# Optimization experiments

Hardware: AMD Instinct MI355X
Metric: run time of the kernel (lower is better)

## Reference

```python
import jax, jax.numpy as jnp
import numpy as np

N_NODES = 50000
N_EDGES = 600000
IN_DIM = 128
HID_DIM = 128
OUT_DIM = 128
N_GRAPHS = 64


def _glorot(key, shape):
    lim = np.sqrt(6.0 / (shape[0] + shape[1]))
    return jax.random.uniform(key, shape, jnp.float32, -lim, lim)


def setup_inputs() -> dict:
    key = jax.random.key(0)
    ks = jax.random.split(key, 8)
    h = jax.random.normal(ks[0], (N_NODES, IN_DIM), jnp.float32)
    src = jax.random.randint(ks[1], (N_EDGES,), 0, N_NODES, jnp.int64)
    dst = jax.random.randint(ks[2], (N_EDGES,), 0, N_NODES, jnp.int64)
    graph_ids = jnp.sort(jax.random.randint(ks[3], (N_NODES,), 0, N_GRAPHS, jnp.int64))
    W1 = _glorot(ks[4], (IN_DIM, HID_DIM)); b1 = jnp.zeros((HID_DIM,), jnp.float32)
    W2 = _glorot(ks[5], (HID_DIM, HID_DIM)); b2 = jnp.zeros((HID_DIM,), jnp.float32)
    W3 = _glorot(ks[6], (HID_DIM, OUT_DIM)); b3 = jnp.zeros((OUT_DIM,), jnp.float32)
    return {"h": h, "src": src, "dst": dst, "graph_ids": graph_ids,
            "W1": W1, "b1": b1, "W2": W2, "b2": b2, "W3": W3, "b3": b3,
            "n_graphs": N_GRAPHS}


def _graph_conv(h, src, dst, norm_src, norm_dst, W, b):
    # DGL GraphConv, norm='both': D_dst^{-1/2} A^T D_src^{-1/2} h W + b
    m = h * norm_src[:, None]                                   # [N, d]
    agg = jax.ops.segment_sum(m[src], dst, num_segments=h.shape[0])  # [N, d]
    return (agg * norm_dst[:, None]) @ W + b


def reference(h, src, dst, graph_ids, W1, b1, W2, b2, W3, b3, n_graphs):
    n = h.shape[0]
    ones = jnp.ones((src.shape[0],), h.dtype)
    out_deg = jnp.clip(jax.ops.segment_sum(ones, src, num_segments=n), 1.0)
    in_deg = jnp.clip(jax.ops.segment_sum(ones, dst, num_segments=n), 1.0)
    norm_src = out_deg ** -0.5
    norm_dst = in_deg ** -0.5

    x = jax.nn.relu(_graph_conv(h, src, dst, norm_src, norm_dst, W1, b1))
    x = jax.nn.relu(_graph_conv(x, src, dst, norm_src, norm_dst, W2, b2))
    x = jax.nn.relu(_graph_conv(x, src, dst, norm_src, norm_dst, W3, b3))

    # dgl.mean_nodes: per-graph mean over nodes
    gsum = jax.ops.segment_sum(x, graph_ids, num_segments=n_graphs)          # [G, d]
    gcnt = jax.ops.segment_sum(jnp.ones((n,), x.dtype), graph_ids, num_segments=n_graphs)
    return gsum / jnp.clip(gcnt, 1.0)[:, None]
```

## Files before the change

kernel.cpp:

```cpp
#include <hip/hip_runtime.h>
#include <hip/hip_fp16.h>


#define DIM 128
#define GRAPHS 64

typedef _Float16 half8 __attribute__((ext_vector_type(8)));
typedef _Float16 half4 __attribute__((ext_vector_type(4)));
typedef float floatx4 __attribute__((ext_vector_type(4)));

#define HIST_R 4
#define HIST_S 64
#define NPR 12500
#define LDSW (NPR / 2)

__global__ __launch_bounds__(256) void k_hist(const int* __restrict__ src,
                                              const int* __restrict__ dst,
                                              unsigned* __restrict__ partial, int E) {
    __shared__ unsigned hist[LDSW];
    int b = blockIdx.x;
    int a = b / (HIST_R * HIST_S);
    int r = (b / HIST_S) % HIST_R;
    int s = b % HIST_S;
    const int* arr = a ? dst : src;
    for (int i = threadIdx.x; i < LDSW; i += 256) hist[i] = 0;
    __syncthreads();
    int chunk = (E + HIST_S - 1) / HIST_S;
    int e0 = s * chunk;
    int e1 = min(e0 + chunk, E);
    unsigned base = (unsigned)(r * NPR);
    for (int i = e0 + threadIdx.x; i < e1; i += 256) {
        unsigned n = (unsigned)arr[i] - base;
        if (n < NPR) atomicAdd(&hist[n >> 1], 1u << ((n & 1) * 16));
    }
    __syncthreads();
    unsigned* outp = partial + ((size_t)(a * HIST_R + r) * HIST_S + s) * LDSW;
    for (int i = threadIdx.x; i < LDSW; i += 256) outp[i] = hist[i];
}

__global__ __launch_bounds__(256) void k_hist_merge(const unsigned* __restrict__ partial,
                                                    float* __restrict__ ns,
                                                    float* __restrict__ nd,
                                                    int* __restrict__ inc,
                                                    int* __restrict__ bsum, int N) {
    __shared__ int sred[256];
    int nb = (N + 255) / 256;
    int isDst = (blockIdx.x < nb) ? 1 : 0;
    int cb = isDst ? blockIdx.x : blockIdx.x - nb;
    int n = cb * 256 + threadIdx.x;
    int deg = 0;
    if (n < N) {
        int a = isDst ? 1 : 0;
        int r = n / NPR;
        int w = (n % NPR) >> 1;
        int field = (n & 1) * 16;
        const unsigned* p = partial + ((size_t)(a * HIST_R + r) * HIST_S) * LDSW + w;
        unsigned sum = 0;
#pragma unroll
        for (int s = 0; s < HIST_S; ++s) sum += p[(size_t)s * LDSW];
        deg = (int)((sum >> field) & 0xFFFFu);
        float nrm = rsqrtf(fmaxf((float)deg, 1.0f));
        if (isDst) { nd[n] = nrm; inc[n] = deg; }
        else       { ns[n] = nrm; }
    }
    if (isDst) {
        sred[threadIdx.x] = deg;
        __syncthreads();
        for (int off = 128; off > 0; off >>= 1) {
            if (threadIdx.x < off) sred[threadIdx.x] += sred[threadIdx.x + off];
            __syncthreads();
        }
        if (threadIdx.x == 0) bsum[cb] = sred[0];
    }
}

__global__ __launch_bounds__(256) void k_scan_write(const int* __restrict__ inc,
                                                    const int* __restrict__ bsum,
                                                    const unsigned* __restrict__ partial,
                                                    int* __restrict__ row_ptr,
                                                    int* __restrict__ cur,
                                                    float* __restrict__ gsum, int N) {
    __shared__ int sb[256];
    __shared__ int s[256];
    __shared__ int exs[256];
    int nb = (N + 255) / 256;
    int t = threadIdx.x;

    int bv = (t < nb) ? bsum[t] : 0;
    sb[t] = bv;
    __syncthreads();
    for (int off = 1; off < 256; off <<= 1) {
        int u = (t >= off) ? sb[t - off] : 0;
        __syncthreads();
        sb[t] += u;
        __syncthreads();
    }
    int excl = sb[t] - bv;
    __syncthreads();
    sb[t] = excl;
    __syncthreads();
    int blockBase = sb[blockIdx.x];

    int B = blockIdx.x * 256;
    int i = B + t;
    int v = (i < N) ? inc[i] : 0;
    s[t] = v;
    __syncthreads();
    for (int off = 1; off < 256; off <<= 1) {
        int u = (t >= off) ? s[t - off] : 0;
        __syncthreads();
        s[t] += u;
        __syncthreads();
    }
    int ex = blockBase + s[t] - v;
    exs[t] = ex;
    if (i < N) row_ptr[i] = ex;
    if (i == N - 1) row_ptr[N] = ex + v;
    if (blockIdx.x == 0) {
        for (int j = t; j < GRAPHS * DIM; j += 256) gsum[j] = 0.0f;
    }
    __syncthreads();

    if (t < 128) {
        int n0 = B + 2 * t;
        if (n0 < N) {
            int r = n0 / NPR;
            int w = (n0 % NPR) >> 1;
            const unsigned* p = partial + ((size_t)(HIST_R + r) * HIST_S) * LDSW + w;
            int run0 = exs[2 * t];
            int run1 = exs[2 * t + 1];
            int* c = cur + (size_t)r * HIST_S * NPR + 2 * w;
#pragma unroll
            for (int sl = 0; sl < HIST_S; ++sl) {
                c[(size_t)sl * NPR + 0] = run0;
                c[(size_t)sl * NPR + 1] = run1;
                unsigned hv = p[(size_t)sl * LDSW];
                run0 += (int)(hv & 0xFFFFu);
                run1 += (int)(hv >> 16);
            }
        }
    }
}

__global__ __launch_bounds__(256) void k_fill2(const int* __restrict__ src,
                                               const int* __restrict__ dst,
                                               const int* __restrict__ cur,
                                               int* __restrict__ csr, int E) {
    __shared__ int lcur[NPR];
    int r = blockIdx.x / HIST_S;
    int s = blockIdx.x % HIST_S;
    const int* cs = cur + (size_t)(r * HIST_S + s) * NPR;
    for (int i = threadIdx.x; i < NPR; i += 256) lcur[i] = cs[i];
    __syncthreads();
    int chunk = (E + HIST_S - 1) / HIST_S;
    int e0 = s * chunk;
    int e1 = min(e0 + chunk, E);
    unsigned base = (unsigned)(r * NPR);
    for (int i = e0 + threadIdx.x; i < e1; i += 256) {
        unsigned d = (unsigned)dst[i] - base;
        if (d < NPR) {
            int p = atomicAdd(&lcur[d], 1);
            csr[p] = src[i];
        }
    }
}

__global__ void k_prep(const float4* __restrict__ h, const float* __restrict__ ns,
                       uint2* __restrict__ A,
                       const float* __restrict__ W1, const float* __restrict__ W2,
                       const float* __restrict__ W3, _Float16* __restrict__ Wt1,
                       _Float16* __restrict__ Wt2, _Float16* __restrict__ Wt3, int N) {
    int i = blockIdx.x * blockDim.x + threadIdx.x;
    int nf4 = N * 32;
    if (i < nf4) {
        int n = i >> 5;
        float s = ns[n];
        float4 v = h[i];
        __half2 p0 = __floats2half2_rn(v.x * s, v.y * s);
        __half2 p1 = __floats2half2_rn(v.z * s, v.w * s);
        uint2 o;
        o.x = *(unsigned*)&p0;
        o.y = *(unsigned*)&p1;
        A[i] = o;
    } else {
        int j = i - nf4;
        if (j < 3 * 16384) {
            int which = j >> 14;
            int local = j & 16383;
            int k = local >> 7;
            int n = local & 127;
            const float* W = (which == 0) ? W1 : (which == 1) ? W2 : W3;
            _Float16* Wt = (which == 0) ? Wt1 : (which == 1) ? Wt2 : Wt3;
            Wt[(size_t)n * DIM + k] = (_Float16)W[local];
        }
    }
}

__global__ __launch_bounds__(256) void k_agg(const uint4* __restrict__ A,
                                             const int* __restrict__ row_ptr,
                                             const int* __restrict__ csr,
                                             const float* __restrict__ nd,
                                             uint4* __restrict__ Bh, int N) {
    int gtid = blockIdx.x * blockDim.x + threadIdx.x;
    int node = gtid >> 6;
    int lane = threadIdx.x & 63;
    if (node >= N) return;
    int e0 = row_ptr[node];
    int e1 = row_ptr[node + 1];
    int grp = lane >> 4;
    int l16 = lane & 15;
    float acc[8];
#pragma unroll
    for (int k = 0; k < 8; ++k) acc[k] = 0.0f;

    for (int base = e0; base < e1; base += 32) {
        int vl = csr[min(base + (lane & 31), e1 - 1)];
        uint4 u[8];
#pragma unroll
        for (int j = 0; j < 8; ++j) {
            int idx = __shfl(vl, 4 * j + grp);
            u[j] = A[(size_t)idx * 16 + l16];
        }
#pragma unroll
        for (int j = 0; j < 8; ++j) {
            if (base + 4 * j + grp < e1) {
                __half2 h0 = *(__half2*)&u[j].x;
                __half2 h1 = *(__half2*)&u[j].y;
                __half2 h2 = *(__half2*)&u[j].z;
                __half2 h3 = *(__half2*)&u[j].w;
                float2 f0 = __half22float2(h0);
                float2 f1 = __half22float2(h1);
                float2 f2 = __half22float2(h2);
                float2 f3 = __half22float2(h3);
                acc[0] += f0.x; acc[1] += f0.y;
                acc[2] += f1.x; acc[3] += f1.y;
                acc[4] += f2.x; acc[5] += f2.y;
                acc[6] += f3.x; acc[7] += f3.y;
            }
        }
    }

#pragma unroll
    for (int k = 0; k < 8; ++k) {
        float v = acc[k];
        v += __shfl_xor(v, 16);
        v += __shfl_xor(v, 32);
        acc[k] = v;
    }

    if (grp == 0) {
        float s = nd[node];
        __half2 p0 = __floats2half2_rn(acc[0] * s, acc[1] * s);
        __half2 p1 = __floats2half2_rn(acc[2] * s, acc[3] * s);
        __half2 p2 = __floats2half2_rn(acc[4] * s, acc[5] * s);
        __half2 p3 = __floats2half2_rn(acc[6] * s, acc[7] * s);
        uint4 o;
        o.x = *(unsigned*)&p0;
        o.y = *(unsigned*)&p1;
        o.z = *(unsigned*)&p2;
        o.w = *(unsigned*)&p3;
        Bh[(size_t)node * 16 + l16] = o;
    }
}

template <bool SCALE_NS>
__global__ __launch_bounds__(256) void k_gemm_t(
    const _Float16* __restrict__ Bin, const _Float16* __restrict__ Wt,
    const float* __restrict__ bias, const float* __restrict__ ns,
    _Float16* __restrict__ Xout, int N) {
    int tid = threadIdx.x;
    int wave = tid >> 6;
    int lane = tid & 63;
    int quad = lane >> 4;
    int l16 = lane & 15;
    int node = blockIdx.x * 64 + wave * 16 + l16;

    half8 b[4];
#pragma unroll
    for (int q = 0; q < 4; ++q) {
        if (node < N) {
            b[q] = *(const half8*)&Bin[(size_t)node * DIM + q * 32 + quad * 8];
        } else {
            b[q] = half8{0, 0, 0, 0, 0, 0, 0, 0};
        }
    }

    floatx4 acc[8];
#pragma unroll
    for (int c = 0; c < 8; ++c) acc[c] = floatx4{0.f, 0.f, 0.f, 0.f};

#pragma unroll
    for (int c = 0; c < 8; ++c) {
#pragma unroll
        for (int q = 0; q < 4; ++q) {
            half8 a = *(const half8*)&Wt[(size_t)(c * 16 + l16) * DIM + q * 32 + quad * 8];
            acc[c] = __builtin_amdgcn_mfma_f32_16x16x32_f16(a, b[q], acc[c], 0, 0, 0);
        }
    }

    if (node < N) {
        float s = SCALE_NS ? ns[node] : 1.0f;
#pragma unroll
        for (int c = 0; c < 8; ++c) {
            float4 b4 = *(const float4*)&bias[c * 16 + quad * 4];
            half4 o;
            o[0] = (_Float16)(fmaxf(acc[c][0] + b4.x, 0.0f) * s);
            o[1] = (_Float16)(fmaxf(acc[c][1] + b4.y, 0.0f) * s);
            o[2] = (_Float16)(fmaxf(acc[c][2] + b4.z, 0.0f) * s);
            o[3] = (_Float16)(fmaxf(acc[c][3] + b4.w, 0.0f) * s);
            *(half4*)&Xout[(size_t)node * DIM + c * 16 + quad * 4] = o;
        }
    }
}

#define PBINS 8
__global__ __launch_bounds__(256) void k_gemm_pool(
    const _Float16* __restrict__ Bin, const _Float16* __restrict__ Wt,
    const float* __restrict__ bias, const int* __restrict__ gid,
    float* __restrict__ gsum, int N) {
    __shared__ float lsum[PBINS * DIM];
    int tid = threadIdx.x;
    for (int i = tid; i < PBINS * DIM; i += 256) lsum[i] = 0.0f;
    int wave = tid >> 6;
    int lane = tid & 63;
    int quad = lane >> 4;
    int l16 = lane & 15;
    int r0 = blockIdx.x * 64;
    int node = r0 + wave * 16 + l16;
    int nodec = min(node, N - 1);

    half8 b[4];
#pragma unroll
    for (int q = 0; q < 4; ++q) {
        if (node < N) {
            b[q] = *(const half8*)&Bin[(size_t)node * DIM + q * 32 + quad * 8];
        } else {
            b[q] = half8{0, 0, 0, 0, 0, 0, 0, 0};
        }
    }

    floatx4 acc[8];
#pragma unroll
    for (int c = 0; c < 8; ++c) acc[c] = floatx4{0.f, 0.f, 0.f, 0.f};
    __syncthreads();

#pragma unroll
    for (int c = 0; c < 8; ++c) {
#pragma unroll
        for (int q = 0; q < 4; ++q) {
            half8 a = *(const half8*)&Wt[(size_t)(c * 16 + l16) * DIM + q * 32 + quad * 8];
            acc[c] = __builtin_amdgcn_mfma_f32_16x16x32_f16(a, b[q], acc[c], 0, 0, 0);
        }
    }

    int g = gid[nodec];
    int g0b = gid[r0];
    int gEb = gid[min(r0 + 63, N - 1)];
    bool ldsPath = (gEb - g0b) < PBINS;
    int gF = __shfl(g, 0);
    int gL = __shfl(g, 15);
    bool uni = (gF == gL);
    float valid = (node < N) ? 1.0f : 0.0f;

#pragma unroll
    for (int c = 0; c < 8; ++c) {
        float4 b4 = *(const float4*)&bias[c * 16 + quad * 4];
        float bv[4] = {b4.x, b4.y, b4.z, b4.w};
#pragma unroll
        for (int r = 0; r < 4; ++r) {
            float v = fmaxf(acc[c][r] + bv[r], 0.0f) * valid;
            int f = c * 16 + quad * 4 + r;
            if (ldsPath) {
                if (uni) {
                    v += __shfl_xor(v, 1);
                    v += __shfl_xor(v, 2);
                    v += __shfl_xor(v, 4);
                    v += __shfl_xor(v, 8);
                    if (l16 == 0) atomicAdd(&lsum[(gF - g0b) * DIM + f], v);
                } else {
                    if (node < N) atomicAdd(&lsum[(g - g0b) * DIM + f], v);
                }
            } else {
                if (node < N) atomicAdd(&gsum[(size_t)g * DIM + f], v);
            }
        }
    }
    __syncthreads();
    if (ldsPath) {
        int ng = gEb - g0b + 1;
        for (int i = tid; i < ng * DIM; i += 256) {
            float sv = lsum[i];
            if (sv != 0.0f) atomicAdd(&gsum[(size_t)g0b * DIM + i], sv);
        }
    }
}

__global__ void k_finalize(const float* __restrict__ gsum, const int* __restrict__ gid,
                           float* __restrict__ out, int N, int G) {
    int i = blockIdx.x * blockDim.x + threadIdx.x;
    if (i < G * DIM) {
        int g = i >> 7;
        int lo = 0, hi = N;
        while (lo < hi) { int m = (lo + hi) >> 1; if (gid[m] < g) lo = m + 1; else hi = m; }
        int lo2 = lo, hi2 = N;
        while (lo2 < hi2) { int m = (lo2 + hi2) >> 1; if (gid[m] < g + 1) lo2 = m + 1; else hi2 = m; }
        float c = fmaxf((float)(lo2 - lo), 1.0f);
        out[i] = gsum[i] / c;
    }
}

extern "C" void kernel_launch(void* const* d_in, const int* in_sizes, int n_in,
                              void* d_out, int out_size, void* d_ws, size_t ws_size,
                              hipStream_t stream) {
    const float* h   = (const float*)d_in[0];
    const int*   src = (const int*)d_in[1];
    const int*   dst = (const int*)d_in[2];
    const int*   gid = (const int*)d_in[3];
    const float* W1  = (const float*)d_in[4];
    const float* b1  = (const float*)d_in[5];
    const float* W2  = (const float*)d_in[6];
    const float* b2  = (const float*)d_in[7];
    const float* W3  = (const float*)d_in[8];
    const float* b3  = (const float*)d_in[9];

    const int N = in_sizes[0] / DIM;
    const int E = in_sizes[1];
    const int G = GRAPHS;
    float* out = (float*)d_out;

    char* ws = (char*)d_ws;
    size_t off = 0;
    auto alloc = [&](size_t bytes) -> void* {
        void* p = ws + off;
        off += (bytes + 255) & ~(size_t)255;
        return p;
    };
    const int nb = (N + 255) / 256;
    uint2* Ah0     = (uint2*)alloc((size_t)N * DIM * 2);
    uint2* Ah1     = (uint2*)alloc((size_t)N * DIM * 2);
    uint2* Bh      = (uint2*)alloc((size_t)N * DIM * 2);
    _Float16* X3   = (_Float16*)alloc((size_t)N * DIM * 2);
    _Float16* Wt1  = (_Float16*)alloc((size_t)DIM * DIM * 2);
    _Float16* Wt2  = (_Float16*)alloc((size_t)DIM * DIM * 2);
    _Float16* Wt3  = (_Float16*)alloc((size_t)DIM * DIM * 2);
    float* ns      = (float*)alloc((size_t)N * 4);
    float* nd      = (float*)alloc((size_t)N * 4);
    int*   inc     = (int*)alloc((size_t)N * 4);
    unsigned* partial = (unsigned*)alloc((size_t)2 * HIST_R * HIST_S * LDSW * 4);
    int*   cur     = (int*)alloc((size_t)HIST_R * HIST_S * NPR * 4);
    int*   row_ptr = (int*)alloc((size_t)(N + 1) * 4);
    int*   csr     = (int*)alloc((size_t)E * 4);
    float* gsum    = (float*)alloc((size_t)G * DIM * 4);
    int*   bsum    = (int*)alloc((size_t)nb * 4);
    (void)X3;

    k_hist<<<2 * HIST_R * HIST_S, 256, 0, stream>>>(src, dst, partial, E);
    k_hist_merge<<<2 * nb, 256, 0, stream>>>(partial, ns, nd, inc, bsum, N);
    k_scan_write<<<nb, 256, 0, stream>>>(inc, bsum, partial, row_ptr, cur, gsum, N);
    k_fill2<<<HIST_R * HIST_S, 256, 0, stream>>>(src, dst, cur, csr, E);

    int prepThreads = N * 32 + 3 * 16384;
    k_prep<<<(prepThreads + 255) / 256, 256, 0, stream>>>((const float4*)h, ns, Ah0,
                                                          W1, W2, W3, Wt1, Wt2, Wt3, N);

    int aggBlocks  = (N * 64 + 255) / 256;
    int gemmBlocks = (N + 63) / 64;

    k_agg<<<aggBlocks, 256, 0, stream>>>((const uint4*)Ah0, row_ptr, csr, nd, (uint4*)Bh, N);
    k_gemm_t<true><<<gemmBlocks, 256, 0, stream>>>((const _Float16*)Bh, Wt1, b1, ns, (_Float16*)Ah1, N);
    k_agg<<<aggBlocks, 256, 0, stream>>>((const uint4*)Ah1, row_ptr, csr, nd, (uint4*)Bh, N);
    k_gemm_t<true><<<gemmBlocks, 256, 0, stream>>>((const _Float16*)Bh, Wt2, b2, ns, (_Float16*)Ah0, N);
    k_agg<<<aggBlocks, 256, 0, stream>>>((const uint4*)Ah0, row_ptr, csr, nd, (uint4*)Bh, N);
    k_gemm_pool<<<gemmBlocks, 256, 0, stream>>>((const _Float16*)Bh, Wt3, b3, gid, gsum, N);

    k_finalize<<<(G * DIM + 255) / 256, 256, 0, stream>>>(gsum, gid, out, N, G);
}
```

Baseline: 310.3 us.

## Split node features into 32-wide slices and aggregate each slice separately

Stores node feature matrices as four feature-slice planes of 32 halves per node, and runs the aggregation kernel once per slice. Each slice's gather working set is a quarter of the full matrix, so the random neighbor reads are intended to hit in L2 more often. The GEMM kernels read and write the sliced layout. In exchange, the edge list and row pointers are read four times, and there are four times as many aggregation launches and waves.

```diff
diff --git a/kernel.cpp b/kernel.cpp
--- a/kernel.cpp
+++ b/kernel.cpp
@@ -174,6 +174,7 @@
     int nf4 = N * 32;
     if (i < nf4) {
         int n = i >> 5;
+        int f4 = i & 31;
         float s = ns[n];
         float4 v = h[i];
         __half2 p0 = __floats2half2_rn(v.x * s, v.y * s);
@@ -181,7 +182,9 @@
         uint2 o;
         o.x = *(unsigned*)&p0;
         o.y = *(unsigned*)&p1;
-        A[i] = o;
+        int q = f4 >> 3;
+        int slot = f4 & 7;
+        A[(size_t)q * N * 8 + (size_t)n * 8 + slot] = o;
     } else {
         int j = i - nf4;
         if (j < 3 * 16384) {
@@ -196,70 +199,54 @@
     }
 }
 
-__global__ __launch_bounds__(256) void k_agg(const uint4* __restrict__ A,
+__global__ __launch_bounds__(256) void k_agg(const uint2* __restrict__ Aq,
                                              const int* __restrict__ row_ptr,
                                              const int* __restrict__ csr,
                                              const float* __restrict__ nd,
-                                             uint4* __restrict__ Bh, int N) {
+                                             uint2* __restrict__ Bq, int N) {
     int gtid = blockIdx.x * blockDim.x + threadIdx.x;
     int node = gtid >> 6;
     int lane = threadIdx.x & 63;
     if (node >= N) return;
     int e0 = row_ptr[node];
     int e1 = row_ptr[node + 1];
-    int grp = lane >> 4;
-    int l16 = lane & 15;
-    float acc[8];
-#pragma unroll
-    for (int k = 0; k < 8; ++k) acc[k] = 0.0f;
+    int grp = lane >> 3;
+    int l8 = lane & 7;
+    float a0 = 0.f, a1 = 0.f, a2 = 0.f, a3 = 0.f;
 
     for (int base = e0; base < e1; base += 32) {
         int vl = csr[min(base + (lane & 31), e1 - 1)];
-        uint4 u[8];
-#pragma unroll
-        for (int j = 0; j < 8; ++j) {
-            int idx = __shfl(vl, 4 * j + grp);
-            u[j] = A[(size_t)idx * 16 + l16];
-        }
-#pragma unroll
-        for (int j = 0; j < 8; ++j) {
-            if (base + 4 * j + grp < e1) {
+        uint2 u[4];
+#pragma unroll
+        for (int j = 0; j < 4; ++j) {
+            int idx = __shfl(vl, 8 * j + grp);
+            u[j] = Aq[(size_t)idx * 8 + l8];
+        }
+#pragma unroll
+        for (int j = 0; j < 4; ++j) {
+            if (base + 8 * j + grp < e1) {
                 __half2 h0 = *(__half2*)&u[j].x;
                 __half2 h1 = *(__half2*)&u[j].y;
-                __half2 h2 = *(__half2*)&u[j].z;
-                __half2 h3 = *(__half2*)&u[j].w;
                 float2 f0 = __half22float2(h0);
                 float2 f1 = __half22float2(h1);
-                float2 f2 = __half22float2(h2);
-                float2 f3 = __half22float2(h3);
-                acc[0] += f0.x; acc[1] += f0.y;
-                acc[2] += f1.x; acc[3] += f1.y;
-                acc[4] += f2.x; acc[5] += f2.y;
-                acc[6] += f3.x; acc[7] += f3.y;
+                a0 += f0.x; a1 += f0.y; a2 += f1.x; a3 += f1.y;
             }
         }
     }
 
-#pragma unroll
-    for (int k = 0; k < 8; ++k) {
-        float v = acc[k];
-        v += __shfl_xor(v, 16);
-        v += __shfl_xor(v, 32);
-        acc[k] = v;
-    }
+    a0 += __shfl_xor(a0, 8);  a0 += __shfl_xor(a0, 16); a0 += __shfl_xor(a0, 32);
+    a1 += __shfl_xor(a1, 8);  a1 += __shfl_xor(a1, 16); a1 += __shfl_xor(a1, 32);
+    a2 += __shfl_xor(a2, 8);  a2 += __shfl_xor(a2, 16); a2 += __shfl_xor(a2, 32);
+    a3 += __shfl_xor(a3, 8);  a3 += __shfl_xor(a3, 16); a3 += __shfl_xor(a3, 32);
 
     if (grp == 0) {
         float s = nd[node];
-        __half2 p0 = __floats2half2_rn(acc[0] * s, acc[1] * s);
-        __half2 p1 = __floats2half2_rn(acc[2] * s, acc[3] * s);
-        __half2 p2 = __floats2half2_rn(acc[4] * s, acc[5] * s);
-        __half2 p3 = __floats2half2_rn(acc[6] * s, acc[7] * s);
-        uint4 o;
+        __half2 p0 = __floats2half2_rn(a0 * s, a1 * s);
+        __half2 p1 = __floats2half2_rn(a2 * s, a3 * s);
+        uint2 o;
         o.x = *(unsigned*)&p0;
         o.y = *(unsigned*)&p1;
-        o.z = *(unsigned*)&p2;
-        o.w = *(unsigned*)&p3;
-        Bh[(size_t)node * 16 + l16] = o;
+        Bq[(size_t)node * 8 + l8] = o;
     }
 }
 
@@ -274,12 +261,13 @@
     int quad = lane >> 4;
     int l16 = lane & 15;
     int node = blockIdx.x * 64 + wave * 16 + l16;
+    size_t QS = (size_t)N * 32;
 
     half8 b[4];
 #pragma unroll
     for (int q = 0; q < 4; ++q) {
         if (node < N) {
-            b[q] = *(const half8*)&Bin[(size_t)node * DIM + q * 32 + quad * 8];
+            b[q] = *(const half8*)&Bin[q * QS + (size_t)node * 32 + quad * 8];
         } else {
             b[q] = half8{0, 0, 0, 0, 0, 0, 0, 0};
         }
@@ -308,7 +296,8 @@
             o[1] = (_Float16)(fmaxf(acc[c][1] + b4.y, 0.0f) * s);
             o[2] = (_Float16)(fmaxf(acc[c][2] + b4.z, 0.0f) * s);
             o[3] = (_Float16)(fmaxf(acc[c][3] + b4.w, 0.0f) * s);
-            *(half4*)&Xout[(size_t)node * DIM + c * 16 + quad * 4] = o;
+            int f0 = c * 16 + quad * 4;
+            *(half4*)&Xout[(f0 >> 5) * QS + (size_t)node * 32 + (f0 & 31)] = o;
         }
     }
 }
@@ -328,12 +317,13 @@
     int r0 = blockIdx.x * 64;
     int node = r0 + wave * 16 + l16;
     int nodec = min(node, N - 1);
+    size_t QS = (size_t)N * 32;
 
     half8 b[4];
 #pragma unroll
     for (int q = 0; q < 4; ++q) {
         if (node < N) {
-            b[q] = *(const half8*)&Bin[(size_t)node * DIM + q * 32 + quad * 8];
+            b[q] = *(const half8*)&Bin[q * QS + (size_t)node * 32 + quad * 8];
         } else {
             b[q] = half8{0, 0, 0, 0, 0, 0, 0, 0};
         }
@@ -439,7 +429,6 @@
     uint2* Ah0     = (uint2*)alloc((size_t)N * DIM * 2);
     uint2* Ah1     = (uint2*)alloc((size_t)N * DIM * 2);
     uint2* Bh      = (uint2*)alloc((size_t)N * DIM * 2);
-    _Float16* X3   = (_Float16*)alloc((size_t)N * DIM * 2);
     _Float16* Wt1  = (_Float16*)alloc((size_t)DIM * DIM * 2);
     _Float16* Wt2  = (_Float16*)alloc((size_t)DIM * DIM * 2);
     _Float16* Wt3  = (_Float16*)alloc((size_t)DIM * DIM * 2);
@@ -452,7 +441,6 @@
     int*   csr     = (int*)alloc((size_t)E * 4);
     float* gsum    = (float*)alloc((size_t)G * DIM * 4);
     int*   bsum    = (int*)alloc((size_t)nb * 4);
-    (void)X3;
 
     k_hist<<<2 * HIST_R * HIST_S, 256, 0, stream>>>(src, dst, partial, E);
     k_hist_merge<<<2 * nb, 256, 0, stream>>>(partial, ns, nd, inc, bsum, N);
@@ -465,12 +453,16 @@
 
     int aggBlocks  = (N * 64 + 255) / 256;
     int gemmBlocks = (N + 63) / 64;
-
-    k_agg<<<aggBlocks, 256, 0, stream>>>((const uint4*)Ah0, row_ptr, csr, nd, (uint4*)Bh, N);
+    size_t QU2 = (size_t)N * 8;
+
+    for (int q = 0; q < 4; ++q)
+        k_agg<<<aggBlocks, 256, 0, stream>>>(Ah0 + q * QU2, row_ptr, csr, nd, Bh + q * QU2, N);
     k_gemm_t<true><<<gemmBlocks, 256, 0, stream>>>((const _Float16*)Bh, Wt1, b1, ns, (_Float16*)Ah1, N);
-    k_agg<<<aggBlocks, 256, 0, stream>>>((const uint4*)Ah1, row_ptr, csr, nd, (uint4*)Bh, N);
+    for (int q = 0; q < 4; ++q)
+        k_agg<<<aggBlocks, 256, 0, stream>>>(Ah1 + q * QU2, row_ptr, csr, nd, Bh + q * QU2, N);
     k_gemm_t<true><<<gemmBlocks, 256, 0, stream>>>((const _Float16*)Bh, Wt2, b2, ns, (_Float16*)Ah0, N);
-    k_agg<<<aggBlocks, 256, 0, stream>>>((const uint4*)Ah0, row_ptr, csr, nd, (uint4*)Bh, N);
+    for (int q = 0; q < 4; ++q)
+        k_agg<<<aggBlocks, 256, 0, stream>>>(Ah0 + q * QU2, row_ptr, csr, nd, Bh + q * QU2, N);
     k_gemm_pool<<<gemmBlocks, 256, 0, stream>>>((const _Float16*)Bh, Wt3, b3, gid, gsum, N);
 
     k_finalize<<<(G * DIM + 255) / 256, 256, 0, stream>>>(gsum, gid, out, N, G);
```

New measurement: 429.8 us. +38.5%, slower.

## Replace LDS-partitioned histogram CSR build with global atomic degree count and fill

Applied to the files above, without the earlier changes.

Swaps the multi-pass, LDS-partitioned degree histogram and per-slice cursor scheme for simple global atomics: one pass counts src and dst degrees, a scan produces row_ptr and a single cursor array, and a fill kernel scatters src indices with global atomicAdd on the cursor. This removes the large partial-histogram and cursor buffers and the 64-way serial cursor writes. In exchange it relies on contended global atomics and makes CSR neighbor order nondeterministic, which may change floating-point summation order and gather locality in the aggregation kernels.

```diff
diff --git a/kernel.cpp b/kernel.cpp
--- a/kernel.cpp
+++ b/kernel.cpp
@@ -9,40 +9,22 @@
 typedef _Float16 half4 __attribute__((ext_vector_type(4)));
 typedef float floatx4 __attribute__((ext_vector_type(4)));
 
-#define HIST_R 4
-#define HIST_S 64
-#define NPR 12500
-#define LDSW (NPR / 2)
-
-__global__ __launch_bounds__(256) void k_hist(const int* __restrict__ src,
-                                              const int* __restrict__ dst,
-                                              unsigned* __restrict__ partial, int E) {
-    __shared__ unsigned hist[LDSW];
-    int b = blockIdx.x;
-    int a = b / (HIST_R * HIST_S);
-    int r = (b / HIST_S) % HIST_R;
-    int s = b % HIST_S;
-    const int* arr = a ? dst : src;
-    for (int i = threadIdx.x; i < LDSW; i += 256) hist[i] = 0;
-    __syncthreads();
-    int chunk = (E + HIST_S - 1) / HIST_S;
-    int e0 = s * chunk;
-    int e1 = min(e0 + chunk, E);
-    unsigned base = (unsigned)(r * NPR);
-    for (int i = e0 + threadIdx.x; i < e1; i += 256) {
-        unsigned n = (unsigned)arr[i] - base;
-        if (n < NPR) atomicAdd(&hist[n >> 1], 1u << ((n & 1) * 16));
-    }
-    __syncthreads();
-    unsigned* outp = partial + ((size_t)(a * HIST_R + r) * HIST_S + s) * LDSW;
-    for (int i = threadIdx.x; i < LDSW; i += 256) outp[i] = hist[i];
-}
-
-__global__ __launch_bounds__(256) void k_hist_merge(const unsigned* __restrict__ partial,
-                                                    float* __restrict__ ns,
-                                                    float* __restrict__ nd,
-                                                    int* __restrict__ inc,
-                                                    int* __restrict__ bsum, int N) {
+__global__ __launch_bounds__(256) void k_deg(const int* __restrict__ src,
+                                             const int* __restrict__ dst,
+                                             int* __restrict__ degs,
+                                             int* __restrict__ degd, int E) {
+    int e = blockIdx.x * 256 + threadIdx.x;
+    if (e < E) {
+        atomicAdd(&degs[src[e]], 1);
+        atomicAdd(&degd[dst[e]], 1);
+    }
+}
+
+__global__ __launch_bounds__(256) void k_bsum(const int* __restrict__ degs,
+                                              const int* __restrict__ degd,
+                                              float* __restrict__ ns,
+                                              float* __restrict__ nd,
+                                              int* __restrict__ bsum, int N) {
     __shared__ int sred[256];
     int nb = (N + 255) / 256;
     int isDst = (blockIdx.x < nb) ? 1 : 0;
@@ -50,18 +32,9 @@
     int n = cb * 256 + threadIdx.x;
     int deg = 0;
     if (n < N) {
-        int a = isDst ? 1 : 0;
-        int r = n / NPR;
-        int w = (n % NPR) >> 1;
-        int field = (n & 1) * 16;
-        const unsigned* p = partial + ((size_t)(a * HIST_R + r) * HIST_S) * LDSW + w;
-        unsigned sum = 0;
-#pragma unroll
-        for (int s = 0; s < HIST_S; ++s) sum += p[(size_t)s * LDSW];
-        deg = (int)((sum >> field) & 0xFFFFu);
+        deg = isDst ? degd[n] : degs[n];
         float nrm = rsqrtf(fmaxf((float)deg, 1.0f));
-        if (isDst) { nd[n] = nrm; inc[n] = deg; }
-        else       { ns[n] = nrm; }
+        if (isDst) nd[n] = nrm; else ns[n] = nrm;
     }
     if (isDst) {
         sred[threadIdx.x] = deg;
@@ -74,15 +47,13 @@
     }
 }
 
-__global__ __launch_bounds__(256) void k_scan_write(const int* __restrict__ inc,
-                                                    const int* __restrict__ bsum,
-                                                    const unsigned* __restrict__ partial,
-                                                    int* __restrict__ row_ptr,
-                                                    int* __restrict__ cur,
-                                                    float* __restrict__ gsum, int N) {
+__global__ __launch_bounds__(256) void k_scan(const int* __restrict__ degd,
+                                              const int* __restrict__ bsum,
+                                              int* __restrict__ row_ptr,
+                                              int* __restrict__ cursor,
+                                              float* __restrict__ gsum, int N) {
     __shared__ int sb[256];
     __shared__ int s[256];
-    __shared__ int exs[256];
     int nb = (N + 255) / 256;
     int t = threadIdx.x;
 
@@ -103,7 +74,7 @@
 
     int B = blockIdx.x * 256;
     int i = B + t;
-    int v = (i < N) ? inc[i] : 0;
+    int v = (i < N) ? degd[i] : 0;
     s[t] = v;
     __syncthreads();
     for (int off = 1; off < 256; off <<= 1) {
@@ -113,55 +84,22 @@
         __syncthreads();
     }
     int ex = blockBase + s[t] - v;
-    exs[t] = ex;
-    if (i < N) row_ptr[i] = ex;
+    if (i < N) { row_ptr[i] = ex; cursor[i] = ex; }
     if (i == N - 1) row_ptr[N] = ex + v;
     if (blockIdx.x == 0) {
         for (int j = t; j < GRAPHS * DIM; j += 256) gsum[j] = 0.0f;
     }
-    __syncthreads();
-
-    if (t < 128) {
-        int n0 = B + 2 * t;
-        if (n0 < N) {
-            int r = n0 / NPR;
-            int w = (n0 % NPR) >> 1;
-            const unsigned* p = partial + ((size_t)(HIST_R + r) * HIST_S) * LDSW + w;
-            int run0 = exs[2 * t];
-            int run1 = exs[2 * t + 1];
-            int* c = cur + (size_t)r * HIST_S * NPR + 2 * w;
-#pragma unroll
-            for (int sl = 0; sl < HIST_S; ++sl) {
-                c[(size_t)sl * NPR + 0] = run0;
-                c[(size_t)sl * NPR + 1] = run1;
-                unsigned hv = p[(size_t)sl * LDSW];
-                run0 += (int)(hv & 0xFFFFu);
-                run1 += (int)(hv >> 16);
-            }
-        }
-    }
-}
-
-__global__ __launch_bounds__(256) void k_fill2(const int* __restrict__ src,
-                                               const int* __restrict__ dst,
-                                               const int* __restrict__ cur,
-                                               int* __restrict__ csr, int E) {
-    __shared__ int lcur[NPR];
-    int r = blockIdx.x / HIST_S;
-    int s = blockIdx.x % HIST_S;
-    const int* cs = cur + (size_t)(r * HIST_S + s) * NPR;
-    for (int i = threadIdx.x; i < NPR; i += 256) lcur[i] = cs[i];
-    __syncthreads();
-    int chunk = (E + HIST_S - 1) / HIST_S;
-    int e0 = s * chunk;
-    int e1 = min(e0 + chunk, E);
-    unsigned base = (unsigned)(r * NPR);
-    for (int i = e0 + threadIdx.x; i < e1; i += 256) {
-        unsigned d = (unsigned)dst[i] - base;
-        if (d < NPR) {
-            int p = atomicAdd(&lcur[d], 1);
-            csr[p] = src[i];
-        }
+}
+
+__global__ __launch_bounds__(256) void k_fill(const int* __restrict__ src,
+                                              const int* __restrict__ dst,
+                                              int* __restrict__ cursor,
+                                              int* __restrict__ csr, int E) {
+    int e = blockIdx.x * 256 + threadIdx.x;
+    if (e < E) {
+        int d = dst[e];
+        int p = atomicAdd(&cursor[d], 1);
+        csr[p] = src[e];
     }
 }
 
@@ -439,25 +377,27 @@
     uint2* Ah0     = (uint2*)alloc((size_t)N * DIM * 2);
     uint2* Ah1     = (uint2*)alloc((size_t)N * DIM * 2);
     uint2* Bh      = (uint2*)alloc((size_t)N * DIM * 2);
-    _Float16* X3   = (_Float16*)alloc((size_t)N * DIM * 2);
     _Float16* Wt1  = (_Float16*)alloc((size_t)DIM * DIM * 2);
     _Float16* Wt2  = (_Float16*)alloc((size_t)DIM * DIM * 2);
     _Float16* Wt3  = (_Float16*)alloc((size_t)DIM * DIM * 2);
     float* ns      = (float*)alloc((size_t)N * 4);
     float* nd      = (float*)alloc((size_t)N * 4);
-    int*   inc     = (int*)alloc((size_t)N * 4);
-    unsigned* partial = (unsigned*)alloc((size_t)2 * HIST_R * HIST_S * LDSW * 4);
-    int*   cur     = (int*)alloc((size_t)HIST_R * HIST_S * NPR * 4);
+    int*   deg2    = (int*)alloc((size_t)2 * N * 4);
     int*   row_ptr = (int*)alloc((size_t)(N + 1) * 4);
+    int*   cursor  = (int*)alloc((size_t)N * 4);
     int*   csr     = (int*)alloc((size_t)E * 4);
     float* gsum    = (float*)alloc((size_t)G * DIM * 4);
     int*   bsum    = (int*)alloc((size_t)nb * 4);
-    (void)X3;
-
-    k_hist<<<2 * HIST_R * HIST_S, 256, 0, stream>>>(src, dst, partial, E);
-    k_hist_merge<<<2 * nb, 256, 0, stream>>>(partial, ns, nd, inc, bsum, N);
-    k_scan_write<<<nb, 256, 0, stream>>>(inc, bsum, partial, row_ptr, cur, gsum, N);
-    k_fill2<<<HIST_R * HIST_S, 256, 0, stream>>>(src, dst, cur, csr, E);
+    int*   degs = deg2;
+    int*   degd = deg2 + N;
+
+    int edgeBlocks = (E + 255) / 256;
+
+    hipMemsetAsync(deg2, 0, (size_t)2 * N * 4, stream);
+    k_deg<<<edgeBlocks, 256, 0, stream>>>(src, dst, degs, degd, E);
+    k_bsum<<<2 * nb, 256, 0, stream>>>(degs, degd, ns, nd, bsum, N);
+    k_scan<<<nb, 256, 0, stream>>>(degd, bsum, row_ptr, cursor, gsum, N);
+    k_fill<<<edgeBlocks, 256, 0, stream>>>(src, dst, cursor, csr, E);
 
     int prepThreads = N * 32 + 3 * 16384;
     k_prep<<<(prepThreads + 255) / 256, 256, 0, stream>>>((const float4*)h, ns, Ah0,
```

Result: slower. 347.3 us (+11.9%).
